# Performance work log

Hardware: AMD Instinct MI355X
Metric: run time of the kernel (lower is better)

## Reference

```python
import jax, jax.numpy as jnp
import numpy as np
from jax import lax

HIDDEN = 10


def setup_inputs() -> dict:
    key = jax.random.key(0)
    ks = jax.random.split(key, 7)
    B, T, I, H, O = 4096, 512, 1, HIDDEN, 1
    return {
        "x": jax.random.normal(ks[0], (B, T, I), dtype=jnp.float32),
        "W_ih": jax.random.normal(ks[1], (4 * H, I), dtype=jnp.float32) * 0.3,
        "W_hh": jax.random.normal(ks[2], (4 * H, H), dtype=jnp.float32) * 0.3,
        "b_ih": jax.random.normal(ks[3], (4 * H,), dtype=jnp.float32) * 0.1,
        "b_hh": jax.random.normal(ks[4], (4 * H,), dtype=jnp.float32) * 0.1,
        "W_fc": jax.random.normal(ks[5], (O, H), dtype=jnp.float32) * 0.3,
        "b_fc": jax.random.normal(ks[6], (O,), dtype=jnp.float32) * 0.1,
    }


def reference(x, W_ih, W_hh, b_ih, b_hh, W_fc, b_fc):
    # x: [B, T, I]; single-layer LSTM (PyTorch gate order i, f, g, o), then
    # Linear on the last timestep's hidden state.
    B = x.shape[0]
    H = W_hh.shape[1]
    b = b_ih + b_hh  # fuse biases once

    def step(carry, xt):
        h, c = carry  # [B, H] each; xt: [B, I]
        gates = xt @ W_ih.T + h @ W_hh.T + b  # [B, 4H]
        i, f, g, o = jnp.split(gates, 4, axis=-1)
        i = jax.nn.sigmoid(i)
        f = jax.nn.sigmoid(f)
        g = jnp.tanh(g)
        o = jax.nn.sigmoid(o)
        c = f * c + i * g
        h = o * jnp.tanh(c)
        return (h, c), None

    h0 = jnp.zeros((B, H), dtype=x.dtype)
    c0 = jnp.zeros((B, H), dtype=x.dtype)
    x_tmajor = jnp.swapaxes(x, 0, 1)  # [T, B, I]
    (h_last, _), _ = lax.scan(step, (h0, c0), x_tmajor)
    return h_last @ W_fc.T + b_fc  # [B, O]
```

## Files before the change

### kernel.cpp

```cpp
#include <hip/hip_runtime.h>


#define NLOG2E (-1.4426950408889634f)

__device__ __forceinline__ float bperm(int byteaddr, float v) {
    return __int_as_float(__builtin_amdgcn_ds_bpermute(byteaddr, __float_as_int(v)));
}

__global__ __launch_bounds__(256, 1) void WeatherLSTM_kernel(
    const float* __restrict__ x,
    const float* __restrict__ W_ih,
    const float* __restrict__ W_hh,
    const float* __restrict__ b_ih,
    const float* __restrict__ b_hh,
    const float* __restrict__ W_fc,
    const float* __restrict__ b_fc,
    float* __restrict__ out,
    int T)
{
    const int tid  = threadIdx.x;
    const int lane = tid & 63;
    const int k    = tid & 15;
    const long e   = (long)blockIdx.x * 16 + (tid >> 4);
    const bool active = (k < 10);

    float whh[4][10], wih[4], bb[4];
    #pragma unroll
    for (int t = 0; t < 4; ++t) {
        const float s = (t == 2) ? (2.0f * NLOG2E) : NLOG2E;
        const int g = t * 10 + k;
        wih[t] = active ? W_ih[g] * s : 0.0f;
        bb[t]  = active ? (b_ih[g] + b_hh[g]) * s : 0.0f;
        #pragma unroll
        for (int j = 0; j < 10; ++j)
            whh[t][j] = active ? W_hh[g * 10 + j] * s : 0.0f;
    }

    float h[10];
    #pragma unroll
    for (int j = 0; j < 10; ++j) h[j] = 0.0f;
    float c = 0.0f, hown = 0.0f;

    const int base = (lane & 48) << 2;
    const float* xe = x + e * (long)T;

    for (int s0 = 0; s0 < T; s0 += 4) {
        const float4 xv = *reinterpret_cast<const float4*>(xe + s0);
        #pragma unroll
        for (int ss = 0; ss < 4; ++ss) {
            const float xt = (&xv.x)[ss];

            float a[4];
            #pragma unroll
            for (int t = 0; t < 4; ++t) {
                float accA = fmaf(xt, wih[t], bb[t]);
                float accB = h[5] * whh[t][5];
                #pragma unroll
                for (int j = 0; j < 5; ++j)
                    accA = fmaf(h[j], whh[t][j], accA);
                #pragma unroll
                for (int j = 6; j < 10; ++j)
                    accB = fmaf(h[j], whh[t][j], accB);
                const float acc = accA + accB;
                const float r = __builtin_amdgcn_rcpf(
                                    1.0f + __builtin_amdgcn_exp2f(acc));
                a[t] = (t == 2) ? fmaf(2.0f, r, -1.0f) : r;
            }

            c = fmaf(a[1], c, a[0] * a[2]);
            const float e2 = __builtin_amdgcn_exp2f(c * (2.0f * NLOG2E));
            hown = a[3] * fmaf(2.0f, __builtin_amdgcn_rcpf(1.0f + e2), -1.0f);

            #pragma unroll
            for (int j = 0; j < 10; ++j)
                h[j] = bperm(base + 4 * j, hown);
        }
    }

    if (k == 0) {
        float o = b_fc[0];
        #pragma unroll
        for (int j = 0; j < 10; ++j)
            o = fmaf(h[j], W_fc[j], o);
        out[e] = o;
    }
}

extern "C" void kernel_launch(void* const* d_in, const int* in_sizes, int n_in,
                              void* d_out, int out_size, void* d_ws, size_t ws_size,
                              hipStream_t stream) {
    const float* x    = (const float*)d_in[0];
    const float* W_ih = (const float*)d_in[1];
    const float* W_hh = (const float*)d_in[2];
    const float* b_ih = (const float*)d_in[3];
    const float* b_hh = (const float*)d_in[4];
    const float* W_fc = (const float*)d_in[5];
    const float* b_fc = (const float*)d_in[6];
    float* out = (float*)d_out;

    const int B = out_size;
    const int T = in_sizes[0] / B;

    dim3 grid(B / 16), block(256);
    hipLaunchKernelGGL(WeatherLSTM_kernel, grid, block, 0, stream,
                       x, W_ih, W_hh, b_ih, b_hh, W_fc, b_fc, out, T);
}
```

Baseline: 104.6 us.

## Split LSTM gates across wave halves with permlane32 swap and LDS hidden broadcast

Each wave now handles two batch elements instead of four. Each 32-lane half computes two of the four gates per hidden unit, and the two halves exchange gate activations through permlane32_swap. The gate nonlinearities and cell update are refactored algebraically to share reciprocals. Hidden state is broadcast through shared memory with vector loads instead of ten ds_bpermute calls, the x loads are prefetched one chunk ahead, and launch bounds allow two blocks per CU with twice as many blocks. Together these shorten the per-step serial dependency chain at the cost of more waves and an LDS write/read round trip per step. The shared-memory handoff relies on wave-synchronous execution with no barrier.

```diff
diff --git a/kernel.cpp b/kernel.cpp
--- a/kernel.cpp
+++ b/kernel.cpp
@@ -3,11 +3,16 @@
 
 #define NLOG2E (-1.4426950408889634f)
 
-__device__ __forceinline__ float bperm(int byteaddr, float v) {
-    return __int_as_float(__builtin_amdgcn_ds_bpermute(byteaddr, __float_as_int(v)));
+typedef float f4v __attribute__((ext_vector_type(4)));
+typedef float f2v __attribute__((ext_vector_type(2)));
+
+__device__ __forceinline__ float swap_rx(float v, bool pick0) {
+    auto r = __builtin_amdgcn_permlane32_swap(
+        __float_as_uint(v), __float_as_uint(v), false, false);
+    return __uint_as_float(pick0 ? r[0] : r[1]);
 }
 
-__global__ __launch_bounds__(256, 1) void WeatherLSTM_kernel(
+__global__ __launch_bounds__(256, 2) void WeatherLSTM_kernel(
     const float* __restrict__ x,
     const float* __restrict__ W_ih,
     const float* __restrict__ W_hh,
@@ -18,66 +23,98 @@
     float* __restrict__ out,
     int T)
 {
+    __shared__ float hsh[8][12];
     const int tid  = threadIdx.x;
     const int lane = tid & 63;
-    const int k    = tid & 15;
-    const long e   = (long)blockIdx.x * 16 + (tid >> 4);
-    const bool active = (k < 10);
+    const int wav  = tid >> 6;
+    const int k    = lane & 15;
+    const int ei   = (lane >> 4) & 1;
+    const int half = lane >> 5;
+    const int eib  = wav * 2 + ei;
+    const long e   = (long)blockIdx.x * 8 + eib;
+    const bool act = (k < 10);
 
-    float whh[4][10], wih[4], bb[4];
+    auto pr = __builtin_amdgcn_permlane32_swap((unsigned)lane, (unsigned)lane,
+                                               false, false);
+    const bool hibc  = (__builtin_amdgcn_readfirstlane((int)pr[0]) == 32);
+    const bool pick0 = ((lane < 32) == hibc);
+
+    const int t0 = 2 * half, t1 = t0 + 1;
+    const float sc0 = (t0 == 2) ? (2.0f * NLOG2E) : NLOG2E;
+    const float sc1 = NLOG2E;
+    const int g0 = t0 * 10 + k, g1 = t1 * 10 + k;
+    float wh0[10], wh1[10];
+    const float wx0 = act ? W_ih[g0] * sc0 : 0.0f;
+    const float wx1 = act ? W_ih[g1] * sc1 : 0.0f;
+    const float bb0 = act ? (b_ih[g0] + b_hh[g0]) * sc0 : 0.0f;
+    const float bb1 = act ? (b_ih[g1] + b_hh[g1]) * sc1 : 0.0f;
     #pragma unroll
-    for (int t = 0; t < 4; ++t) {
-        const float s = (t == 2) ? (2.0f * NLOG2E) : NLOG2E;
-        const int g = t * 10 + k;
-        wih[t] = active ? W_ih[g] * s : 0.0f;
-        bb[t]  = active ? (b_ih[g] + b_hh[g]) * s : 0.0f;
-        #pragma unroll
-        for (int j = 0; j < 10; ++j)
-            whh[t][j] = active ? W_hh[g * 10 + j] * s : 0.0f;
+    for (int j = 0; j < 10; ++j) {
+        wh0[j] = act ? W_hh[g0 * 10 + j] * sc0 : 0.0f;
+        wh1[j] = act ? W_hh[g1 * 10 + j] * sc1 : 0.0f;
     }
+
+    float* hrow = &hsh[eib][0];
+    const bool writeok = (half == 1) && act;
+    float* wptr = hrow + (writeok ? k : 10);
 
     float h[10];
     #pragma unroll
     for (int j = 0; j < 10; ++j) h[j] = 0.0f;
-    float c = 0.0f, hown = 0.0f;
+    float c = 0.0f;
 
-    const int base = (lane & 48) << 2;
     const float* xe = x + e * (long)T;
-
-    for (int s0 = 0; s0 < T; s0 += 4) {
-        const float4 xv = *reinterpret_cast<const float4*>(xe + s0);
+    f4v xv = *reinterpret_cast<const f4v*>(xe);
+    for (int s0i = 0; s0i < T; s0i += 4) {
+        const int snext = (s0i + 4 < T) ? (s0i + 4) : s0i;
+        const f4v xnext = *reinterpret_cast<const f4v*>(xe + snext);
         #pragma unroll
         for (int ss = 0; ss < 4; ++ss) {
-            const float xt = (&xv.x)[ss];
+            const float xt = xv[ss];
 
-            float a[4];
+            float a0A = fmaf(xt, wx0, bb0);
+            float a1A = fmaf(xt, wx1, bb1);
+            float a0B = h[5] * wh0[5];
+            float a1B = h[5] * wh1[5];
             #pragma unroll
-            for (int t = 0; t < 4; ++t) {
-                float accA = fmaf(xt, wih[t], bb[t]);
-                float accB = h[5] * whh[t][5];
-                #pragma unroll
-                for (int j = 0; j < 5; ++j)
-                    accA = fmaf(h[j], whh[t][j], accA);
-                #pragma unroll
-                for (int j = 6; j < 10; ++j)
-                    accB = fmaf(h[j], whh[t][j], accB);
-                const float acc = accA + accB;
-                const float r = __builtin_amdgcn_rcpf(
-                                    1.0f + __builtin_amdgcn_exp2f(acc));
-                a[t] = (t == 2) ? fmaf(2.0f, r, -1.0f) : r;
+            for (int j = 0; j < 5; ++j) {
+                a0A = fmaf(h[j], wh0[j], a0A);
+                a1A = fmaf(h[j], wh1[j], a1A);
             }
+            #pragma unroll
+            for (int j = 6; j < 10; ++j) {
+                a0B = fmaf(h[j], wh0[j], a0B);
+                a1B = fmaf(h[j], wh1[j], a1B);
+            }
+            const float p0 = __builtin_amdgcn_exp2f(a0A + a0B);
+            const float p1 = __builtin_amdgcn_exp2f(a1A + a1B);
 
-            c = fmaf(a[1], c, a[0] * a[2]);
-            const float e2 = __builtin_amdgcn_exp2f(c * (2.0f * NLOG2E));
-            hown = a[3] * fmaf(2.0f, __builtin_amdgcn_rcpf(1.0f + e2), -1.0f);
+            const float s0 = swap_rx(p0, pick0);
 
-            #pragma unroll
-            for (int j = 0; j < 10; ++j)
-                h[j] = bperm(base + 4 * j, hown);
+            const float qa = 1.0f + p0, qb = 1.0f + p1;
+            const float qs = 1.0f + s0, m  = 1.0f - s0;
+            const float A   = qa * qs;
+            const float num = fmaf(c, A, m * qb);
+            c = num * __builtin_amdgcn_rcpf(A * qb);
+            const float pc = __builtin_amdgcn_exp2f(c * (2.0f * NLOG2E));
+
+            const float s1 = swap_rx(pc, pick0);
+
+            const float qc = 1.0f + s1, mc = 1.0f - s1;
+            const float hown = mc * __builtin_amdgcn_rcpf(qb * qc);
+
+            *wptr = hown;
+            const f4v r0 = *reinterpret_cast<const f4v*>(hrow);
+            const f4v r1 = *reinterpret_cast<const f4v*>(hrow + 4);
+            const f2v r2 = *reinterpret_cast<const f2v*>(hrow + 8);
+            h[0] = r0[0]; h[1] = r0[1]; h[2] = r0[2]; h[3] = r0[3];
+            h[4] = r1[0]; h[5] = r1[1]; h[6] = r1[2]; h[7] = r1[3];
+            h[8] = r2[0]; h[9] = r2[1];
         }
+        xv = xnext;
     }
 
-    if (k == 0) {
+    if (half == 0 && k == 0) {
         float o = b_fc[0];
         #pragma unroll
         for (int j = 0; j < 10; ++j)
@@ -101,7 +138,7 @@
     const int B = out_size;
     const int T = in_sizes[0] / B;
 
-    dim3 grid(B / 16), block(256);
+    dim3 grid(B / 8), block(256);
     hipLaunchKernelGGL(WeatherLSTM_kernel, grid, block, 0, stream,
                        x, W_ih, W_hh, b_ih, b_hh, W_fc, b_fc, out, T);
 }
```

Measured after the change: 121.5 us. +16.1%, slower.
